# Kernel tuning notes

Hardware: AMD Instinct MI355X
Metric: run time of the kernel (lower is better)

The kernel has to match this reference:

```python
import jax, jax.numpy as jnp
import numpy as np


def setup_inputs() -> dict:
    key = jax.random.key(0)
    ks = jax.random.split(key, 5)
    B, S, D, F, E = 4, 4096, 512, 2048, 8
    scale = 0.02
    return {
        "x": jax.random.normal(ks[0], (B, S, D), dtype=jnp.float32),
        "gate_w": jax.random.normal(ks[1], (E, D), dtype=jnp.float32) * scale,
        "w1": jax.random.normal(ks[2], (E, F, D), dtype=jnp.float32) * scale,
        "w2": jax.random.normal(ks[3], (E, D, F), dtype=jnp.float32) * scale,
        "w3": jax.random.normal(ks[4], (E, F, D), dtype=jnp.float32) * scale,
        "top_k": 2,
    }


def _moe(x, gate_w, w1, w2, w3, top_k):
    B, S, D = x.shape
    E = gate_w.shape[0]
    xt = x.reshape(-1, D)                       # [T, D], T = B*S
    T = xt.shape[0]

    # --- router: softmax in float32, top-k, renormalize (matches Mixtral) ---
    logits = xt @ gate_w.T                      # [T, E]
    probs = jax.nn.softmax(logits.astype(jnp.float32), axis=-1)
    rw, sel = jax.lax.top_k(probs, top_k)       # [T, k], [T, k]
    rw = rw / jnp.sum(rw, axis=-1, keepdims=True)
    rw = rw.astype(x.dtype)

    # dense combine weights [T, E]: zero for unselected experts
    combine = jnp.zeros((T, E), dtype=x.dtype)
    combine = combine.at[jnp.arange(T)[:, None], sel].add(rw)

    # --- per-expert SwiGLU-style FFN (relu gate), combined by routing weights ---
    out = jnp.zeros_like(xt)
    for e in range(E):  # small fixed expert count
        h = jax.nn.relu(xt @ w1[e].T) * (xt @ w3[e].T)   # [T, F]
        out = out + combine[:, e:e + 1] * (h @ w2[e].T)  # [T, D]
    return out.reshape(B, S, D)


def reference(x, gate_w, w1, w2, w3, top_k):
    return _moe(x, gate_w, w1, w2, w3, top_k)
```

## Files before the change

### kernel.cpp

```cpp
#include <hip/hip_runtime.h>
#include <stdint.h>

#define T_TOK 16384
#define D_DIM 512
#define F_DIM 2048
#define E_NUM 8
#define MAXR  33792

typedef __bf16 bf16x8 __attribute__((ext_vector_type(8)));
typedef float  f32x4  __attribute__((ext_vector_type(4)));

__device__ __forceinline__ unsigned short f2b(float f) {
  union { float f; unsigned u; } a; a.f = f;
  unsigned u = a.u;
  u = u + 0x7fffu + ((u >> 16) & 1u);
  return (unsigned short)(u >> 16);
}
__device__ __forceinline__ float b2f(unsigned short h) {
  union { unsigned u; float f; } a; a.u = ((unsigned)h) << 16;
  return a.f;
}
__device__ __forceinline__ void load_lds16(const void* g, void* l) {
  __builtin_amdgcn_global_load_lds(
      (const __attribute__((address_space(1))) void*)g,
      (__attribute__((address_space(3))) void*)l, 16, 0, 0);
}

#define CSTRIDE 16

__global__ __launch_bounds__(256) void router_kernel(
    const float* __restrict__ x, const float* __restrict__ gw,
    int* __restrict__ sel, float* __restrict__ rw)
{
  int lane = threadIdx.x & 63;
  int wid  = threadIdx.x >> 6;
  int t = blockIdx.x * 4 + wid;
  const float4* xp = (const float4*)(x + (size_t)t * D_DIM + lane * 8);
  float4 a0 = xp[0], a1 = xp[1];
  float lg[E_NUM];
#pragma unroll
  for (int e = 0; e < E_NUM; ++e) {
    const float4* gp = (const float4*)(gw + (size_t)e * D_DIM + lane * 8);
    float4 g0 = gp[0], g1 = gp[1];
    float s = a0.x*g0.x + a0.y*g0.y + a0.z*g0.z + a0.w*g0.w
            + a1.x*g1.x + a1.y*g1.y + a1.z*g1.z + a1.w*g1.w;
#pragma unroll
    for (int off = 32; off; off >>= 1) s += __shfl_xor(s, off);
    lg[e] = s;
  }
  if (lane == 0) {
    int i0 = 0; float m0 = lg[0];
#pragma unroll
    for (int e = 1; e < E_NUM; ++e) if (lg[e] > m0) { m0 = lg[e]; i0 = e; }
    int i1 = -1; float m1 = -1e30f;
#pragma unroll
    for (int e = 0; e < E_NUM; ++e) if (e != i0 && lg[e] > m1) { m1 = lg[e]; i1 = e; }
    float w0 = 1.0f / (1.0f + expf(m1 - m0));
    sel[2*t] = i0; sel[2*t+1] = i1;
    rw[2*t] = w0;  rw[2*t+1] = 1.0f - w0;
  }
}

__global__ __launch_bounds__(256) void hist_kernel(
    const int* __restrict__ sel, int* __restrict__ counts)
{
  __shared__ int h[E_NUM];
  if (threadIdx.x < E_NUM) h[threadIdx.x] = 0;
  __syncthreads();
  int t = blockIdx.x * 256 + threadIdx.x;
  int e0 = sel[2*t], e1 = sel[2*t+1];
  atomicAdd(&h[e0], 1);
  atomicAdd(&h[e1], 1);
  __syncthreads();
  if (threadIdx.x < E_NUM) atomicAdd(&counts[threadIdx.x * CSTRIDE], h[threadIdx.x]);
}

__global__ void scan_kernel(const int* __restrict__ counts, int* __restrict__ offs,
    int* __restrict__ padTot, int* __restrict__ ptok,
    float* __restrict__ pw, int* __restrict__ pexp)
{
  if (threadIdx.x != 0 || blockIdx.x != 0) return;
  int o = 0;
  for (int e = 0; e < E_NUM; ++e) {
    offs[e] = o;
    int c = counts[e * CSTRIDE];
    int padded = (c + 127) & ~127;
    for (int i = c; i < padded; ++i) { ptok[o+i] = 0; pw[o+i] = 0.0f; pexp[o+i] = e; }
    o += padded;
  }
  *padTot = o;
}

__global__ __launch_bounds__(256) void assign_kernel(
    const int* __restrict__ sel, const float* __restrict__ rw,
    const int* __restrict__ offs, int* __restrict__ cursor,
    int* __restrict__ ptok, float* __restrict__ pw, int* __restrict__ pexp,
    int* __restrict__ t2s)
{
  __shared__ int lcnt[E_NUM];
  __shared__ int base[E_NUM];
  if (threadIdx.x < E_NUM) lcnt[threadIdx.x] = 0;
  __syncthreads();
  int t = blockIdx.x * 256 + threadIdx.x;
  int e[2], rank[2];
  float w[2];
#pragma unroll
  for (int k = 0; k < 2; ++k) {
    e[k] = sel[2*t+k];
    w[k] = rw[2*t+k];
    rank[k] = atomicAdd(&lcnt[e[k]], 1);
  }
  __syncthreads();
  if (threadIdx.x < E_NUM)
    base[threadIdx.x] = atomicAdd(&cursor[threadIdx.x * CSTRIDE], lcnt[threadIdx.x]);
  __syncthreads();
#pragma unroll
  for (int k = 0; k < 2; ++k) {
    int slot = offs[e[k]] + base[e[k]] + rank[k];
    ptok[slot] = t; pw[slot] = w[k]; pexp[slot] = e[k];
    t2s[2*t+k] = slot;
  }
}

__global__ __launch_bounds__(256) void cvt4_kernel(
    const float* __restrict__ s0, const float* __restrict__ s1,
    const float* __restrict__ s2, const float* __restrict__ s3,
    unsigned short* __restrict__ d0, unsigned short* __restrict__ d1,
    unsigned short* __restrict__ d2, unsigned short* __restrict__ d3)
{
  int seg = blockIdx.x >> 13;
  int i = (blockIdx.x & 8191) * 256 + threadIdx.x;
  const float* s = seg == 0 ? s0 : seg == 1 ? s1 : seg == 2 ? s2 : s3;
  unsigned short* d = seg == 0 ? d0 : seg == 1 ? d1 : seg == 2 ? d2 : d3;
  float4 v = ((const float4*)s)[i];
  ushort4 o;
  o.x = f2b(v.x); o.y = f2b(v.y); o.z = f2b(v.z); o.w = f2b(v.w);
  ((ushort4*)d)[i] = o;
}


__global__ __launch_bounds__(256) void ffn_h_kernel(
    const unsigned short* __restrict__ xb, const unsigned short* __restrict__ w1b,
    const unsigned short* __restrict__ w3b, const int* __restrict__ ptok,
    const int* __restrict__ pexp, const int* __restrict__ padTot,
    unsigned short* __restrict__ H)
{
  __shared__ unsigned short As[128 * 64];
  __shared__ unsigned short B1s[64 * 64];
  __shared__ unsigned short B3s[64 * 64];
  const int NTN = F_DIM / 64;
  int tm = blockIdx.x / NTN;
  int tn = blockIdx.x % NTN;
  int row0 = tm * 128;
  if (row0 >= *padTot) return;
  int e  = pexp[row0];
  int f0 = tn * 64;
  const unsigned short* W1 = w1b + (size_t)e * F_DIM * D_DIM;
  const unsigned short* W3 = w3b + (size_t)e * F_DIM * D_DIM;
  int lane = threadIdx.x & 63;
  int wid  = threadIdx.x >> 6;
  int wm = wid >> 1, wn = wid & 1;
  int sub  = lane >> 3;
  int colSw = (((lane & 7) ^ sub) * 8);
  int xs = (lane & 7) << 3;

  int tok[4];
#pragma unroll
  for (int c = 0; c < 4; ++c) tok[c] = ptok[row0 + (wid*4 + c)*8 + sub];

  f32x4 acc1[4][2] = {};
  f32x4 acc3[4][2] = {};

  for (int k0 = 0; k0 < D_DIM; k0 += 64) {
#pragma unroll
    for (int c = 0; c < 4; ++c)
      load_lds16(xb + (size_t)tok[c]*D_DIM + k0 + colSw, &As[(wid*4 + c)*512 + lane*8]);
#pragma unroll
    for (int c = 0; c < 2; ++c) {
      int fr = (wid*2 + c)*8 + sub;
      load_lds16(W1 + (size_t)(f0 + fr)*D_DIM + k0 + colSw, &B1s[(wid*2 + c)*512 + lane*8]);
      load_lds16(W3 + (size_t)(f0 + fr)*D_DIM + k0 + colSw, &B3s[(wid*2 + c)*512 + lane*8]);
    }
    __syncthreads();
#pragma unroll
    for (int kk = 0; kk < 64; kk += 32) {
      int cphys = (kk + ((lane >> 4) << 3)) ^ xs;
      bf16x8 af[4], b1f[2], b3f[2];
#pragma unroll
      for (int mt = 0; mt < 4; ++mt)
        af[mt] = *(const bf16x8*)&As[(wm*64 + mt*16 + (lane&15))*64 + cphys];
#pragma unroll
      for (int nt = 0; nt < 2; ++nt) {
        b1f[nt] = *(const bf16x8*)&B1s[(wn*32 + nt*16 + (lane&15))*64 + cphys];
        b3f[nt] = *(const bf16x8*)&B3s[(wn*32 + nt*16 + (lane&15))*64 + cphys];
      }
#pragma unroll
      for (int mt = 0; mt < 4; ++mt)
#pragma unroll
        for (int nt = 0; nt < 2; ++nt) {
          acc1[mt][nt] = __builtin_amdgcn_mfma_f32_16x16x32_bf16(af[mt], b1f[nt], acc1[mt][nt], 0, 0, 0);
          acc3[mt][nt] = __builtin_amdgcn_mfma_f32_16x16x32_bf16(af[mt], b3f[nt], acc3[mt][nt], 0, 0, 0);
        }
    }
    __syncthreads();
  }
#pragma unroll
  for (int mt = 0; mt < 4; ++mt) {
    int rbase = row0 + wm*64 + mt*16 + (lane>>4)*4;
#pragma unroll
    for (int nt = 0; nt < 2; ++nt) {
      int col = f0 + wn*32 + nt*16 + (lane & 15);
#pragma unroll
      for (int j = 0; j < 4; ++j) {
        float h = fmaxf(acc1[mt][nt][j], 0.0f) * acc3[mt][nt][j];
        H[(size_t)(rbase + j) * F_DIM + col] = f2b(h);
      }
    }
  }
}

__global__ __launch_bounds__(256) void ffn_out_kernel(
    const unsigned short* __restrict__ H, const unsigned short* __restrict__ w2b,
    const int* __restrict__ pexp, const float* __restrict__ pw,
    const int* __restrict__ padTot, unsigned short* __restrict__ contrib)
{
  __shared__ unsigned short As[128 * 64];
  __shared__ unsigned short Bs[128 * 64];
  int tm = blockIdx.x >> 2;
  int tn = blockIdx.x & 3;
  int row0 = tm * 128;
  if (row0 >= *padTot) return;
  int e  = pexp[row0];
  int d0 = tn * 128;
  const unsigned short* W2 = w2b + (size_t)e * D_DIM * F_DIM;
  int lane = threadIdx.x & 63;
  int wid  = threadIdx.x >> 6;
  int wm = wid >> 1, wn = wid & 1;
  int sub  = lane >> 3;
  int colSw = (((lane & 7) ^ sub) * 8);
  int xs = (lane & 7) << 3;

  f32x4 acc[4][4] = {};

  for (int k0 = 0; k0 < F_DIM; k0 += 64) {
#pragma unroll
    for (int c = 0; c < 4; ++c) {
      int r = (wid*4 + c)*8 + sub;
      load_lds16(H  + (size_t)(row0 + r)*F_DIM + k0 + colSw, &As[(wid*4 + c)*512 + lane*8]);
      load_lds16(W2 + (size_t)(d0   + r)*F_DIM + k0 + colSw, &Bs[(wid*4 + c)*512 + lane*8]);
    }
    __syncthreads();
#pragma unroll
    for (int kk = 0; kk < 64; kk += 32) {
      int cphys = (kk + ((lane >> 4) << 3)) ^ xs;
      bf16x8 af[4], bf[4];
#pragma unroll
      for (int mt = 0; mt < 4; ++mt)
        af[mt] = *(const bf16x8*)&As[(wm*64 + mt*16 + (lane&15))*64 + cphys];
#pragma unroll
      for (int nt = 0; nt < 4; ++nt)
        bf[nt] = *(const bf16x8*)&Bs[(wn*64 + nt*16 + (lane&15))*64 + cphys];
#pragma unroll
      for (int mt = 0; mt < 4; ++mt)
#pragma unroll
        for (int nt = 0; nt < 4; ++nt)
          acc[mt][nt] = __builtin_amdgcn_mfma_f32_16x16x32_bf16(af[mt], bf[nt], acc[mt][nt], 0, 0, 0);
    }
    __syncthreads();
  }
#pragma unroll
  for (int mt = 0; mt < 4; ++mt) {
    int rbase = row0 + wm*64 + mt*16 + (lane>>4)*4;
    float sw[4];
#pragma unroll
    for (int j = 0; j < 4; ++j) sw[j] = pw[rbase + j];
#pragma unroll
    for (int nt = 0; nt < 4; ++nt) {
      int col = d0 + wn*64 + nt*16 + (lane & 15);
#pragma unroll
      for (int j = 0; j < 4; ++j)
        contrib[(size_t)(rbase + j) * D_DIM + col] = f2b(acc[mt][nt][j] * sw[j]);
    }
  }
}

__global__ __launch_bounds__(256) void combine_kernel(
    const unsigned short* __restrict__ contrib, const int* __restrict__ t2s,
    float* __restrict__ out)
{
  int i = blockIdx.x * 256 + threadIdx.x;
  int t = i >> 7;
  int c = (i & 127) * 4;
  int s0 = t2s[2*t], s1 = t2s[2*t+1];
  ushort4 u0 = *(const ushort4*)&contrib[(size_t)s0 * D_DIM + c];
  ushort4 u1 = *(const ushort4*)&contrib[(size_t)s1 * D_DIM + c];
  float4 o;
  o.x = b2f(u0.x) + b2f(u1.x);
  o.y = b2f(u0.y) + b2f(u1.y);
  o.z = b2f(u0.z) + b2f(u1.z);
  o.w = b2f(u0.w) + b2f(u1.w);
  *(float4*)&out[(size_t)t * D_DIM + c] = o;
}

#define OFF_SEL   ((size_t)2048)
#define OFF_RW    (OFF_SEL  + (size_t)2*T_TOK*4)
#define OFF_T2S   (OFF_RW   + (size_t)2*T_TOK*4)
#define OFF_PTOK  (OFF_T2S  + (size_t)2*T_TOK*4)
#define OFF_PW    (OFF_PTOK + (size_t)MAXR*4)
#define OFF_PEXP  (OFF_PW   + (size_t)MAXR*4)
#define OFF_XB    (OFF_PEXP + (size_t)MAXR*4)
#define OFF_W1B   (OFF_XB   + (size_t)T_TOK*D_DIM*2)
#define OFF_W3B   (OFF_W1B  + (size_t)E_NUM*F_DIM*D_DIM*2)
#define OFF_W2B   (OFF_W3B  + (size_t)E_NUM*F_DIM*D_DIM*2)
#define OFF_H     (OFF_W2B  + (size_t)E_NUM*F_DIM*D_DIM*2)
#define OFF_CONTR (OFF_H    + (size_t)MAXR*F_DIM*2)

extern "C" void kernel_launch(void* const* d_in, const int* in_sizes, int n_in,
                              void* d_out, int out_size, void* d_ws, size_t ws_size,
                              hipStream_t stream) {
  const float* x  = (const float*)d_in[0];
  const float* gw = (const float*)d_in[1];
  const float* w1 = (const float*)d_in[2];
  const float* w2 = (const float*)d_in[3];
  const float* w3 = (const float*)d_in[4];
  float* out = (float*)d_out;
  char* ws = (char*)d_ws;

  int*   counts = (int*)(ws + 0);
  int*   cursor = (int*)(ws + 512);
  int*   offs   = (int*)(ws + 1024);
  int*   padTot = (int*)(ws + 1056);
  int*   sel    = (int*)(ws + OFF_SEL);
  float* rw     = (float*)(ws + OFF_RW);
  int*   t2s    = (int*)(ws + OFF_T2S);
  int*   ptok   = (int*)(ws + OFF_PTOK);
  float* pw     = (float*)(ws + OFF_PW);
  int*   pexp   = (int*)(ws + OFF_PEXP);
  unsigned short* xb      = (unsigned short*)(ws + OFF_XB);
  unsigned short* w1b     = (unsigned short*)(ws + OFF_W1B);
  unsigned short* w3b     = (unsigned short*)(ws + OFF_W3B);
  unsigned short* w2b     = (unsigned short*)(ws + OFF_W2B);
  unsigned short* Hbuf    = (unsigned short*)(ws + OFF_H);
  unsigned short* contrib = (unsigned short*)(ws + OFF_CONTR);

  hipMemsetAsync(ws, 0, 2048, stream);

  cvt4_kernel<<<4 * 8192, 256, 0, stream>>>(x, w1, w3, w2, xb, w1b, w3b, w2b);

  router_kernel<<<T_TOK/4, 256, 0, stream>>>(x, gw, sel, rw);
  hist_kernel<<<T_TOK/256, 256, 0, stream>>>(sel, counts);
  scan_kernel<<<1, 64, 0, stream>>>(counts, offs, padTot, ptok, pw, pexp);
  assign_kernel<<<T_TOK/256, 256, 0, stream>>>(sel, rw, offs, cursor, ptok, pw, pexp, t2s);

  ffn_h_kernel<<<(MAXR/128)*(F_DIM/64), 256, 0, stream>>>(xb, w1b, w3b, ptok, pexp, padTot, Hbuf);
  ffn_out_kernel<<<(MAXR/128)*(D_DIM/128), 256, 0, stream>>>(Hbuf, w2b, pexp, pw, padTot, contrib);
  combine_kernel<<<(T_TOK*D_DIM/4)/256, 256, 0, stream>>>(contrib, t2s, out);

  (void)in_sizes; (void)n_in; (void)out_size; (void)ws_size;
}
```

Measured before the change: 386.2 us.

## Rewrite gate/up FFN GEMM as 256x128 double-buffered 8-wave pipelined kernel

Replaces the 128x64-tile gate/up GEMM with a 512-thread kernel using 256x128 tiles, double-buffered LDS, and a hand-interleaved schedule. Global-to-LDS loads are overlapped with MFMA work using explicit vmcnt waits and barriers. Expert padding grows to 256 rows to match the new tile height, which adds some wasted rows. The contrib buffer now aliases the x bf16 buffer to save workspace. The larger tile raises reuse of weights and activations, at the cost of higher register and LDS pressure and more padding.

```diff
diff --git a/kernel.cpp b/kernel.cpp
--- a/kernel.cpp
+++ b/kernel.cpp
@@ -5,7 +5,7 @@
 #define D_DIM 512
 #define F_DIM 2048
 #define E_NUM 8
-#define MAXR  33792
+#define MAXR  34816
 
 typedef __bf16 bf16x8 __attribute__((ext_vector_type(8)));
 typedef float  f32x4  __attribute__((ext_vector_type(4)));
@@ -68,9 +68,8 @@
   if (threadIdx.x < E_NUM) h[threadIdx.x] = 0;
   __syncthreads();
   int t = blockIdx.x * 256 + threadIdx.x;
-  int e0 = sel[2*t], e1 = sel[2*t+1];
-  atomicAdd(&h[e0], 1);
-  atomicAdd(&h[e1], 1);
+  atomicAdd(&h[sel[2*t]], 1);
+  atomicAdd(&h[sel[2*t+1]], 1);
   __syncthreads();
   if (threadIdx.x < E_NUM) atomicAdd(&counts[threadIdx.x * CSTRIDE], h[threadIdx.x]);
 }
@@ -84,7 +83,7 @@
   for (int e = 0; e < E_NUM; ++e) {
     offs[e] = o;
     int c = counts[e * CSTRIDE];
-    int padded = (c + 127) & ~127;
+    int padded = (c + 255) & ~255;
     for (int i = c; i < padded; ++i) { ptok[o+i] = 0; pw[o+i] = 0.0f; pexp[o+i] = e; }
     o += padded;
   }
@@ -139,80 +138,137 @@
 }
 
 
-__global__ __launch_bounds__(256) void ffn_h_kernel(
+__device__ __forceinline__ void stageA8(unsigned short* dst, const unsigned short* xb,
+    const int* tokr, int kt, int half, int tid, int csw) {
+  int k0 = kt * 64;
+#pragma unroll
+  for (int r = 0; r < 2; ++r) {
+    int h = half*2 + r;
+    int rl = h*64 + (tid>>3);
+    load_lds16(xb + (size_t)tokr[h]*D_DIM + k0 + csw, &dst[rl*64 + (tid&7)*8]);
+  }
+}
+__device__ __forceinline__ void stageB8(unsigned short* dst, const unsigned short* W,
+    int f0, int kt, int tid, int csw) {
+  int k0 = kt * 64;
+#pragma unroll
+  for (int r = 0; r < 2; ++r) {
+    int rl = r*64 + (tid>>3);
+    load_lds16(W + (size_t)(f0+rl)*D_DIM + k0 + csw, &dst[rl*64 + (tid&7)*8]);
+  }
+}
+__device__ __forceinline__ void readA8(bf16x8 (*af)[2], const unsigned short* buf,
+    int wm, int lane, int xs, int mlo) {
+#pragma unroll
+  for (int m = 0; m < 4; ++m)
+#pragma unroll
+    for (int s = 0; s < 2; ++s)
+      af[m][s] = *(const bf16x8*)&buf[(wm*128 + (mlo+m)*16 + (lane&15))*64 + ((s*32 + ((lane>>4)<<3)) ^ xs)];
+}
+__device__ __forceinline__ void readB8(bf16x8 (*bf)[2], const unsigned short* buf,
+    int wn, int lane, int xs) {
+#pragma unroll
+  for (int n = 0; n < 2; ++n)
+#pragma unroll
+    for (int s = 0; s < 2; ++s)
+      bf[n][s] = *(const bf16x8*)&buf[(wn*32 + n*16 + (lane&15))*64 + ((s*32 + ((lane>>4)<<3)) ^ xs)];
+}
+__device__ __forceinline__ void mfmaq(f32x4 (*acc)[2], const bf16x8 (*af)[2], const bf16x8 (*bf)[2]) {
+#pragma unroll
+  for (int m = 0; m < 4; ++m)
+#pragma unroll
+    for (int n = 0; n < 2; ++n)
+#pragma unroll
+      for (int s = 0; s < 2; ++s)
+        acc[m][n] = __builtin_amdgcn_mfma_f32_16x16x32_bf16(af[m][s], bf[n][s], acc[m][n], 0, 0, 0);
+}
+#define BAR() __builtin_amdgcn_s_barrier()
+#define VMC6() do { asm volatile("s_waitcnt vmcnt(6)" ::: "memory"); \
+                    __builtin_amdgcn_sched_barrier(0); } while (0)
+
+__global__ __launch_bounds__(512, 2) void ffn_h8_kernel(
     const unsigned short* __restrict__ xb, const unsigned short* __restrict__ w1b,
     const unsigned short* __restrict__ w3b, const int* __restrict__ ptok,
     const int* __restrict__ pexp, const int* __restrict__ padTot,
     unsigned short* __restrict__ H)
 {
-  __shared__ unsigned short As[128 * 64];
-  __shared__ unsigned short B1s[64 * 64];
-  __shared__ unsigned short B3s[64 * 64];
-  const int NTN = F_DIM / 64;
-  int tm = blockIdx.x / NTN;
-  int tn = blockIdx.x % NTN;
-  int row0 = tm * 128;
+  __shared__ unsigned short As0[256*64], As1[256*64];
+  __shared__ unsigned short B1s0[128*64], B1s1[128*64];
+  __shared__ unsigned short B3s0[128*64], B3s1[128*64];
+  int tm = blockIdx.x >> 4;
+  int tn = blockIdx.x & 15;
+  int row0 = tm * 256;
   if (row0 >= *padTot) return;
   int e  = pexp[row0];
-  int f0 = tn * 64;
+  int f0 = tn * 128;
   const unsigned short* W1 = w1b + (size_t)e * F_DIM * D_DIM;
   const unsigned short* W3 = w3b + (size_t)e * F_DIM * D_DIM;
-  int lane = threadIdx.x & 63;
-  int wid  = threadIdx.x >> 6;
-  int wm = wid >> 1, wn = wid & 1;
-  int sub  = lane >> 3;
-  int colSw = (((lane & 7) ^ sub) * 8);
-  int xs = (lane & 7) << 3;
-
-  int tok[4];
-#pragma unroll
-  for (int c = 0; c < 4; ++c) tok[c] = ptok[row0 + (wid*4 + c)*8 + sub];
-
-  f32x4 acc1[4][2] = {};
-  f32x4 acc3[4][2] = {};
-
-  for (int k0 = 0; k0 < D_DIM; k0 += 64) {
-#pragma unroll
-    for (int c = 0; c < 4; ++c)
-      load_lds16(xb + (size_t)tok[c]*D_DIM + k0 + colSw, &As[(wid*4 + c)*512 + lane*8]);
-#pragma unroll
-    for (int c = 0; c < 2; ++c) {
-      int fr = (wid*2 + c)*8 + sub;
-      load_lds16(W1 + (size_t)(f0 + fr)*D_DIM + k0 + colSw, &B1s[(wid*2 + c)*512 + lane*8]);
-      load_lds16(W3 + (size_t)(f0 + fr)*D_DIM + k0 + colSw, &B3s[(wid*2 + c)*512 + lane*8]);
-    }
-    __syncthreads();
-#pragma unroll
-    for (int kk = 0; kk < 64; kk += 32) {
-      int cphys = (kk + ((lane >> 4) << 3)) ^ xs;
-      bf16x8 af[4], b1f[2], b3f[2];
-#pragma unroll
-      for (int mt = 0; mt < 4; ++mt)
-        af[mt] = *(const bf16x8*)&As[(wm*64 + mt*16 + (lane&15))*64 + cphys];
-#pragma unroll
-      for (int nt = 0; nt < 2; ++nt) {
-        b1f[nt] = *(const bf16x8*)&B1s[(wn*32 + nt*16 + (lane&15))*64 + cphys];
-        b3f[nt] = *(const bf16x8*)&B3s[(wn*32 + nt*16 + (lane&15))*64 + cphys];
-      }
-#pragma unroll
-      for (int mt = 0; mt < 4; ++mt)
-#pragma unroll
-        for (int nt = 0; nt < 2; ++nt) {
-          acc1[mt][nt] = __builtin_amdgcn_mfma_f32_16x16x32_bf16(af[mt], b1f[nt], acc1[mt][nt], 0, 0, 0);
-          acc3[mt][nt] = __builtin_amdgcn_mfma_f32_16x16x32_bf16(af[mt], b3f[nt], acc3[mt][nt], 0, 0, 0);
-        }
-    }
-    __syncthreads();
-  }
-#pragma unroll
-  for (int mt = 0; mt < 4; ++mt) {
-    int rbase = row0 + wm*64 + mt*16 + (lane>>4)*4;
-#pragma unroll
-    for (int nt = 0; nt < 2; ++nt) {
-      int col = f0 + wn*32 + nt*16 + (lane & 15);
+  int tid  = threadIdx.x;
+  int lane = tid & 63;
+  int wid  = tid >> 6;
+  int wm = wid >> 2, wn = wid & 3;
+  int xs  = (lane & 7) << 3;
+  int csw = ((tid & 7) ^ ((tid >> 3) & 7)) * 8;
+
+  int tokr[4];
+#pragma unroll
+  for (int h = 0; h < 4; ++h) tokr[h] = ptok[row0 + h*64 + (tid>>3)];
+
+  f32x4 acc1[8][2] = {};
+  f32x4 acc3[8][2] = {};
+  bf16x8 afL[4][2], afH[4][2], b1f[2][2], b3f[2][2];
+
+  stageB8(B1s0, W1, f0, 0, tid, csw);
+  stageA8(As0, xb, tokr, 0, 0, tid, csw);
+  stageA8(As0, xb, tokr, 0, 1, tid, csw);
+  stageB8(B3s0, W3, f0, 0, tid, csw);
+  stageB8(B1s1, W1, f0, 1, tid, csw);
+  stageA8(As1, xb, tokr, 1, 0, tid, csw);
+  stageA8(As1, xb, tokr, 1, 1, tid, csw);
+  VMC6();
+  BAR();
+
+  for (int i = 0; i < 4; ++i) {
+    int ktB = 2*i + 1;
+    int s2 = (2*i + 2 < 8) ? 2*i + 2 : 6;
+    int s3 = (2*i + 3 < 8) ? 2*i + 3 : 7;
+    readA8(afL, As0, wm, lane, xs, 0);
+    readB8(b1f, B1s0, wn, lane, xs);
+    stageB8(B3s1, W3, f0, ktB, tid, csw);
+    BAR(); mfmaq(&acc1[0], afL, b1f); BAR();
+    readA8(afH, As0, wm, lane, xs, 4);
+    stageB8(B1s0, W1, f0, s2, tid, csw);
+    BAR(); mfmaq(&acc1[4], afH, b1f); BAR();
+    readB8(b3f, B3s0, wn, lane, xs);
+    stageA8(As0, xb, tokr, s2, 0, tid, csw);
+    BAR(); mfmaq(&acc3[0], afL, b3f); BAR();
+    stageA8(As0, xb, tokr, s2, 1, tid, csw);
+    VMC6();
+    BAR(); mfmaq(&acc3[4], afH, b3f); BAR();
+    readA8(afL, As1, wm, lane, xs, 0);
+    readB8(b1f, B1s1, wn, lane, xs);
+    stageB8(B3s0, W3, f0, s2, tid, csw);
+    BAR(); mfmaq(&acc1[0], afL, b1f); BAR();
+    readA8(afH, As1, wm, lane, xs, 4);
+    stageB8(B1s1, W1, f0, s3, tid, csw);
+    BAR(); mfmaq(&acc1[4], afH, b1f); BAR();
+    readB8(b3f, B3s1, wn, lane, xs);
+    stageA8(As1, xb, tokr, s3, 0, tid, csw);
+    BAR(); mfmaq(&acc3[0], afL, b3f); BAR();
+    stageA8(As1, xb, tokr, s3, 1, tid, csw);
+    VMC6();
+    BAR(); mfmaq(&acc3[4], afH, b3f); BAR();
+  }
+
+#pragma unroll
+  for (int mi = 0; mi < 8; ++mi) {
+    int rbase = row0 + wm*128 + mi*16 + (lane>>4)*4;
+#pragma unroll
+    for (int ni = 0; ni < 2; ++ni) {
+      int col = f0 + wn*32 + ni*16 + (lane & 15);
 #pragma unroll
       for (int j = 0; j < 4; ++j) {
-        float h = fmaxf(acc1[mt][nt][j], 0.0f) * acc3[mt][nt][j];
+        float h = fmaxf(acc1[mi][ni][j], 0.0f) * acc3[mi][ni][j];
         H[(size_t)(rbase + j) * F_DIM + col] = f2b(h);
       }
     }
@@ -313,7 +369,7 @@
 #define OFF_W3B   (OFF_W1B  + (size_t)E_NUM*F_DIM*D_DIM*2)
 #define OFF_W2B   (OFF_W3B  + (size_t)E_NUM*F_DIM*D_DIM*2)
 #define OFF_H     (OFF_W2B  + (size_t)E_NUM*F_DIM*D_DIM*2)
-#define OFF_CONTR (OFF_H    + (size_t)MAXR*F_DIM*2)
+#define OFF_CONTR OFF_XB
 
 extern "C" void kernel_launch(void* const* d_in, const int* in_sizes, int n_in,
                               void* d_out, int out_size, void* d_ws, size_t ws_size,
@@ -352,7 +408,7 @@
   scan_kernel<<<1, 64, 0, stream>>>(counts, offs, padTot, ptok, pw, pexp);
   assign_kernel<<<T_TOK/256, 256, 0, stream>>>(sel, rw, offs, cursor, ptok, pw, pexp, t2s);
 
-  ffn_h_kernel<<<(MAXR/128)*(F_DIM/64), 256, 0, stream>>>(xb, w1b, w3b, ptok, pexp, padTot, Hbuf);
+  ffn_h8_kernel<<<(MAXR/256)*(F_DIM/128), 512, 0, stream>>>(xb, w1b, w3b, ptok, pexp, padTot, Hbuf);
   ffn_out_kernel<<<(MAXR/128)*(D_DIM/128), 256, 0, stream>>>(Hbuf, w2b, pexp, pw, padTot, contrib);
   combine_kernel<<<(T_TOK*D_DIM/4)/256, 256, 0, stream>>>(contrib, t2s, out);
 
```

Result: faster. 376.7 us (-2.4%).
